# Performance work log

Hardware: AMD Instinct MI355X
Metric: run time of the kernel (lower is better)

The kernel has to match this reference:

```python
import math
import jax, jax.numpy as jnp
import numpy as np
from jax import lax

CELL_SIZE = 8
N_BINS = 9
SIGNED = False


def _conv3x3(x, k):
    # x: [N,1,H,W], k: [1,1,3,3]; padding=1 (SAME), stride 1
    return lax.conv_general_dilated(
        x, k, window_strides=(1, 1), padding=[(1, 1), (1, 1)],
        dimension_numbers=("NCHW", "OIHW", "NCHW"))


def setup_inputs() -> dict:
    key = jax.random.key(0)
    x = jax.random.uniform(key, (64, 1, 512, 512), dtype=jnp.float32)
    sobel_x = jnp.array([[-1., 0., 1.], [-2., 0., 2.], [-1., 0., 1.]],
                        dtype=jnp.float32).reshape(1, 1, 3, 3)
    sobel_y = jnp.array([[-1., -2., -1.], [0., 0., 0.], [1., 2., 1.]],
                        dtype=jnp.float32).reshape(1, 1, 3, 3)
    return {"x": x, "sobel_x": sobel_x, "sobel_y": sobel_y}


def reference(x, sobel_x, sobel_y):
    n, _, H, W = x.shape
    angle_range = 2 * math.pi if SIGNED else math.pi

    gx = _conv3x3(x, sobel_x)  # [N,1,H,W]
    gy = _conv3x3(x, sobel_y)
    mag = jnp.sqrt(gx * gx + gy * gy)          # [N,1,H,W]
    ang = jnp.arctan2(gx, gy)                  # note: atan2(gx, gy) as in source
    ang = ang + math.pi if SIGNED else jnp.abs(ang)
    bins = jnp.floor(ang / angle_range * (N_BINS - 1)).astype(jnp.int32)  # [N,1,H,W]

    # scatter_(dim=1): one-hot write of magnitudes into bin channel
    onehot = jax.nn.one_hot(bins[:, 0], N_BINS, axis=1, dtype=mag.dtype)  # [N,nb,H,W]
    out = onehot * mag                                                     # [N,nb,H,W]

    # AvgPool2d(cell,stride=cell) * cell**2 == sum over each cell
    cs = CELL_SIZE
    hog = out.reshape(n, N_BINS, H // cs, cs, W // cs, cs).sum(axis=(3, 5))
    return hog.reshape(-1)
```

## Files before the change

### kernel.cpp

```cpp
#include <hip/hip_runtime.h>
#include <math.h>

#define IMG_H 512
#define IMG_W 512
#define NB 9

__global__ __launch_bounds__(256, 4) void hog_kernel(const float* __restrict__ x,
                                                     float* __restrict__ out) {
#pragma clang fp contract(off)
    const int tid = threadIdx.x;
    const int cx = tid & 63;
    const int cy = (blockIdx.x << 2) + (tid >> 6);
    const int n  = blockIdx.y;

    const float* img = x + (size_t)n * (IMG_H * IMG_W);
    const int x0 = cx << 3;
    const int y0 = cy << 3;

    float a[10], b[10], c[10];
    float acc[NB];
#pragma unroll
    for (int k = 0; k < NB; ++k) acc[k] = 0.0f;

    auto load_row = [&](float* r, int y) {
        if (y < 0 || y >= IMG_H) {
#pragma unroll
            for (int i = 0; i < 10; ++i) r[i] = 0.0f;
            return;
        }
        const float* row = img + (size_t)y * IMG_W;
        const float4 p0 = *(const float4*)(row + x0);
        const float4 p1 = *(const float4*)(row + x0 + 4);
        r[1] = p0.x; r[2] = p0.y; r[3] = p0.z; r[4] = p0.w;
        r[5] = p1.x; r[6] = p1.y; r[7] = p1.z; r[8] = p1.w;
        r[0] = (x0 == 0)         ? 0.0f : row[x0 - 1];
        r[9] = (x0 + 8 >= IMG_W) ? 0.0f : row[x0 + 8];
    };

    load_row(a, y0 - 1);
    load_row(b, y0);

    const float PI_F = 3.14159274101257324f;
    const float T1F  = 0.41421356237309503f;
    const float T3F  = 2.41421356237309503f;
    const float KPI  = 2.54647909f;
    const float EPS  = 5e-5f;

#pragma unroll
    for (int ry = 0; ry < 8; ++ry) {
        load_row(c, y0 + ry + 1);

#pragma unroll
        for (int j = 0; j < 8; ++j) {
            const float A0 = a[j], A1 = a[j + 1], A2 = a[j + 2];
            const float B0 = b[j], B2 = b[j + 2];
            const float C0 = c[j], C1 = c[j + 1], C2 = c[j + 2];

            const float gx = ((-A0 + (A2 - 2.0f * B0)) + (2.0f * B2 - C0)) + C2;
            const float gy = (((-A0 - 2.0f * A1) + (-A2)) + (C0 + 2.0f * C1)) + C2;

            const float u = fabsf(gx);
            const float W = fabsf(gy);
            const float q = u * u + W * W;
            const float mag = sqrtf(q);

            const float b1 = W * T1F;
            const float b3 = W * T3F;
            const int cnt = (int)(u > b1) + (int)(u > b3) + (int)(u > W);
            int bin = (gy > 0.0f) ? cnt : 7 - cnt;
            float wA = mag;

            const float KW = KPI * W;
            const float E  = EPS * q;
            const bool flag = (fabsf(u - b1) * KW < E) |
                              (fabsf(u - b3) * KW < E) |
                              (fabsf(u - W)  * KW < E) |
                              (u * KW < E);

            if (flag) {
                const float angf = (float)atan2((double)u, (double)gy);
                const float tc = (float)((double)angf / (double)PI_F) * 8.0f;
                int bc = (int)tc;
                bin = bc > 8 ? 8 : bc;
                const float tn = roundf(tc);
                const int B = (int)tn;
                if (B >= 1 && B <= 8 && fabsf(tc - tn) < 4e-6f &&
                    mag <= 1.05f) {
                    const float hw = 0.5f * mag;
                    bin = B - 1; wA = hw;
#pragma unroll
                    for (int k = 0; k < NB; ++k)
                        acc[k] += (k == B) ? hw : 0.0f;
                }
            }

#pragma unroll
            for (int k = 0; k < NB; ++k)
                acc[k] += (bin == k) ? wA : 0.0f;
        }

#pragma unroll
        for (int i = 0; i < 10; ++i) { a[i] = b[i]; b[i] = c[i]; }
    }

    float* o = out + (size_t)n * (NB * 64 * 64) + (size_t)cy * 64 + cx;
#pragma unroll
    for (int k = 0; k < NB; ++k) o[(size_t)k * 4096] = acc[k];
}

extern "C" void kernel_launch(void* const* d_in, const int* in_sizes, int n_in,
                              void* d_out, int out_size, void* d_ws, size_t ws_size,
                              hipStream_t stream) {
    const float* x = (const float*)d_in[0];
    float* out = (float*)d_out;
    hog_kernel<<<dim3(16, 64, 1), dim3(256, 1, 1), 0, stream>>>(x, out);
}
```

Baseline: 127.8 us.

## Split each HOG cell across two half-waves and combine with a lane shuffle

Each 8x8 cell is now processed by two threads, each handling four rows, and their partial histograms are combined with a cross-half-wave shuffle. The grid doubles to 32x64 blocks and launch bounds are raised to request eight blocks per CU, which increases thread-level parallelism and shortens each thread's serial loop. The exactness-check condition is reduced to a single min-based compare, and bin 8 is handled only in the rare slow path so the common path accumulates eight bins instead of nine. The costs are redundant halo-row loads for each half, a shuffle, and split output writes, and the higher occupancy target may pressure registers.

```diff
diff --git a/kernel.cpp b/kernel.cpp
--- a/kernel.cpp
+++ b/kernel.cpp
@@ -5,17 +5,22 @@
 #define IMG_W 512
 #define NB 9
 
-__global__ __launch_bounds__(256, 4) void hog_kernel(const float* __restrict__ x,
+__global__ __launch_bounds__(256, 8) void hog_kernel(const float* __restrict__ x,
                                                      float* __restrict__ out) {
 #pragma clang fp contract(off)
-    const int tid = threadIdx.x;
-    const int cx = tid & 63;
-    const int cy = (blockIdx.x << 2) + (tid >> 6);
+    const int tid  = threadIdx.x;
+    const int w    = tid >> 6;
+    const int lane = tid & 63;
+    const int cl   = lane & 31;
+    const int half = lane >> 5;
+
+    const int cx = ((w & 1) << 5) | cl;
+    const int cy = (blockIdx.x << 1) | (w >> 1);
     const int n  = blockIdx.y;
 
     const float* img = x + (size_t)n * (IMG_H * IMG_W);
     const int x0 = cx << 3;
-    const int y0 = cy << 3;
+    const int y0 = (cy << 3) + (half << 2);
 
     float a[10], b[10], c[10];
     float acc[NB];
@@ -47,7 +52,7 @@
     const float EPS  = 5e-5f;
 
 #pragma unroll
-    for (int ry = 0; ry < 8; ++ry) {
+    for (int ry = 0; ry < 4; ++ry) {
         load_row(c, y0 + ry + 1);
 
 #pragma unroll
@@ -72,12 +77,10 @@
 
             const float KW = KPI * W;
             const float E  = EPS * q;
-            const bool flag = (fabsf(u - b1) * KW < E) |
-                              (fabsf(u - b3) * KW < E) |
-                              (fabsf(u - W)  * KW < E) |
-                              (u * KW < E);
+            const float md = fminf(fminf(fabsf(u - b1), fabsf(u - b3)),
+                                   fminf(fabsf(u - W), u));
 
-            if (flag) {
+            if (md * KW < E) {
                 const float angf = (float)atan2((double)u, (double)gy);
                 const float tc = (float)((double)angf / (double)PI_F) * 8.0f;
                 int bc = (int)tc;
@@ -92,10 +95,14 @@
                     for (int k = 0; k < NB; ++k)
                         acc[k] += (k == B) ? hw : 0.0f;
                 }
+                if (bin == 8) {
+                    acc[8] += wA;
+                    wA = 0.0f; bin = 0;
+                }
             }
 
 #pragma unroll
-            for (int k = 0; k < NB; ++k)
+            for (int k = 0; k < 8; ++k)
                 acc[k] += (bin == k) ? wA : 0.0f;
         }
 
@@ -103,9 +110,18 @@
         for (int i = 0; i < 10; ++i) { a[i] = b[i]; b[i] = c[i]; }
     }
 
+#pragma unroll
+    for (int k = 0; k < NB; ++k)
+        acc[k] += __shfl_xor(acc[k], 32, 64);
+
     float* o = out + (size_t)n * (NB * 64 * 64) + (size_t)cy * 64 + cx;
+    if (half == 0) {
 #pragma unroll
-    for (int k = 0; k < NB; ++k) o[(size_t)k * 4096] = acc[k];
+        for (int k = 0; k < 5; ++k) o[(size_t)k * 4096] = acc[k];
+    } else {
+#pragma unroll
+        for (int k = 5; k < NB; ++k) o[(size_t)k * 4096] = acc[k];
+    }
 }
 
 extern "C" void kernel_launch(void* const* d_in, const int* in_sizes, int n_in,
@@ -113,5 +129,5 @@
                               hipStream_t stream) {
     const float* x = (const float*)d_in[0];
     float* out = (float*)d_out;
-    hog_kernel<<<dim3(16, 64, 1), dim3(256, 1, 1), 0, stream>>>(x, out);
+    hog_kernel<<<dim3(32, 64, 1), dim3(256, 1, 1), 0, stream>>>(x, out);
 }
```

Measured after the change: 157.8 us. +23.4%, slower.
